# Kernel tuning notes

Hardware: AMD Instinct MI355X
Metric: run time of the kernel (lower is better)

The kernel has to match this reference:

```python
import jax, jax.numpy as jnp
import numpy as np

B, CIN, HW_IN = 128, 3, 32
CONV_OUT, CK = 256, 9
NCAPS, PC, PK, PS = 32, 8, 9, 2
NCAT, DOUT = 10, 16
ROUTING_ITERS = 3
DN = ('NCHW', 'OIHW', 'NCHW')


def setup_inputs() -> dict:
    key = jax.random.key(0)
    ks = jax.random.split(key, 6)
    return {
        "x": jax.random.normal(ks[0], (B, CIN, HW_IN, HW_IN), jnp.float32),
        "conv_w": jax.random.normal(ks[1], (CONV_OUT, CIN, CK, CK), jnp.float32) * 0.05,
        "conv_b": jax.random.normal(ks[2], (CONV_OUT,), jnp.float32) * 0.05,
        "prim_w": jax.random.normal(ks[3], (NCAPS, PC, CONV_OUT, PK, PK), jnp.float32) * 0.05,
        "prim_b": jax.random.normal(ks[4], (NCAPS, PC), jnp.float32) * 0.05,
        "dig_w": jax.random.normal(ks[5], (NCAT, 8 * 8 * NCAPS, PC, DOUT), jnp.float32) * 0.05,
    }


def squash(v):
    s = jnp.sum(v * v, axis=-1, keepdims=True)
    return v * (jnp.sqrt(s) / (1.0 + s))


def reference(x, conv_w, conv_b, prim_w, prim_b, dig_w):
    b = x.shape[0]
    # conv + leaky_relu  -> [B, 256, 24, 24]
    h = jax.lax.conv_general_dilated(x, conv_w, (1, 1), 'VALID', dimension_numbers=DN)
    h = jax.nn.leaky_relu(h + conv_b[None, :, None, None])
    # all 32 primary-cap convs as one conv with 32*8 output channels
    w2 = prim_w.reshape(NCAPS * PC, CONV_OUT, PK, PK)
    p = jax.lax.conv_general_dilated(h, w2, (PS, PS), 'VALID', dimension_numbers=DN)
    p = p + prim_b.reshape(-1)[None, :, None, None]          # [B, 32*8, 8, 8]
    hp, wp = p.shape[2], p.shape[3]
    p = p.reshape(b, NCAPS, PC, hp * wp)                      # [B, 32, 8, HW]
    # torch: cat over caps at dim3 -> [B, 8, HW, 32] -> view(B,8,-1) -> transpose(1,2)
    u = p.transpose(0, 3, 1, 2).reshape(b, hp * wp * NCAPS, PC)
    # note: torch flatten order is (HW, cap); transpose(0,2,3,1) gives [B,8,HW,32]
    u = p.transpose(0, 2, 3, 1).reshape(b, PC, hp * wp * NCAPS).transpose(0, 2, 1)
    u = squash(u)                                             # [B, nodes, 8]
    uhat = jnp.einsum('bni,cnid->bcnd', u, dig_w)             # [B, cat, nodes, dout]
    logits = jnp.zeros(uhat.shape[:3] + (1,), uhat.dtype)
    for _ in range(ROUTING_ITERS):
        probs = jax.nn.softmax(logits, axis=1)
        out = squash(jnp.sum(uhat * probs, axis=2))           # [B, cat, dout]
        logits = logits + jnp.sum(uhat * out[:, :, None, :], axis=3, keepdims=True)
    probs = jax.nn.softmax(logits, axis=1)
    return squash(jnp.sum(uhat * probs, axis=2))              # [B, cat, dout]
```

## Files before the change

kernel.cpp:

```cpp
#include <hip/hip_runtime.h>
#include <hip/hip_bf16.h>

typedef __attribute__((ext_vector_type(8))) short bf16x8;
typedef __attribute__((ext_vector_type(4))) float f32x4;
typedef unsigned short ushort_t;

__device__ inline ushort_t f2bf(float f){
    union { float f; unsigned int u; } v; v.f = f;
    unsigned int r = v.u + 0x7fffu + ((v.u >> 16) & 1u);
    return (ushort_t)(r >> 16);
}

__device__ inline void gload_lds16(const void* g, void* l){
    __builtin_amdgcn_global_load_lds(
        (const __attribute__((address_space(1))) unsigned int*)g,
        (__attribute__((address_space(3))) unsigned int*)l, 16, 0, 0);
}

__global__ __launch_bounds__(256) void k_w2t(const float* __restrict__ pw, ushort_t* __restrict__ w2t)
{
    __shared__ float tile[5184];
    const int oc  = blockIdx.x >> 2;
    const int ic0 = (blockIdx.x & 3) * 64;
    const float* src = pw + (oc*256 + ic0)*81;
    for (int j = threadIdx.x; j < 5184; j += 256) tile[j] = src[j];
    __syncthreads();
    for (int j = threadIdx.x; j < 5184; j += 256){
        int p = j >> 6, ic = j & 63;
        w2t[(oc*81 + p)*256 + ic0 + ic] = f2bf(tile[ic*81 + p]);
    }
}

__global__ __launch_bounds__(256) void k_cwb(const float* __restrict__ cw, ushort_t* __restrict__ cwb){
    const int oc = blockIdx.x;
    const int k  = threadIdx.x;
    cwb[oc*256 + k] = (k < 243) ? f2bf(cw[oc*243 + k]) : (ushort_t)0;
}

__global__ __launch_bounds__(256) void k_conv1m(const float* __restrict__ x,
    const ushort_t* __restrict__ cwb, const float* __restrict__ conv_b,
    ushort_t* __restrict__ ht)
{
    __shared__ ushort_t At[8192];
    __shared__ ushort_t Bt[8192];
    const int tid = threadIdx.x;
    const int bid = blockIdx.x;
    const int mt = bid >> 1, nt = bid & 1;
    const int m0 = mt*128, n0 = nt*128;
    const int lane = tid & 63, wave = tid >> 6;
    const int wm = (wave >> 1)*64, wn = (wave & 1)*64;
    const int l16 = lane & 15, lq = lane >> 4;
    const int rx = l16 & 7;

    int xbase[4], aoff[4], swz[4];
    const ushort_t* bsrc[4];
    #pragma unroll
    for (int t=0;t<4;t++){
        const int cid = tid + t*256;
        const int row = cid >> 3, co = cid & 7;
        swz[t] = (row*8 + (co ^ (row & 7)))*8;
        aoff[t] = co*8;
        const int m = m0 + row;
        const int b = m / 576, rem = m - b*576;
        const int oy = rem / 24, ox = rem - oy*24;
        xbase[t] = b*3072 + oy*32 + ox;
        bsrc[t] = cwb + (n0 + row)*256 + co*8;
    }

    f32x4 acc[4][4];
    #pragma unroll
    for (int i=0;i<4;i++)
        #pragma unroll
        for (int j=0;j<4;j++) acc[i][j] = 0;

    for (int step = 0; step < 4; step++){
        const int k0 = step*64;
        #pragma unroll
        for (int t=0;t<4;t++){
            union { ushort_t u[8]; bf16x8 v; } pk;
            #pragma unroll
            for (int j=0;j<8;j++){
                const int k = k0 + aoff[t] + j;
                float val = 0.f;
                if (k < 243){
                    const int ic = k / 81, p = k - ic*81;
                    const int ky = p / 9, kx = p - ky*9;
                    val = x[xbase[t] + ic*1024 + ky*32 + kx];
                }
                pk.u[j] = f2bf(val);
            }
            *(bf16x8*)&At[swz[t]] = pk.v;
        }
        #pragma unroll
        for (int t=0;t<4;t++){
            bf16x8 v = *(const bf16x8*)(bsrc[t] + k0);
            *(bf16x8*)&Bt[swz[t]] = v;
        }
        __syncthreads();
        #pragma unroll
        for (int kk=0; kk<2; kk++){
            bf16x8 a[4], bb[4];
            const int cs = ((kk*4 + lq) ^ rx)*8;
            #pragma unroll
            for (int f=0; f<4; f++){
                a[f]  = *(const bf16x8*)&At[(wm + f*16 + l16)*64 + cs];
                bb[f] = *(const bf16x8*)&Bt[(wn + f*16 + l16)*64 + cs];
            }
            #pragma unroll
            for (int i=0;i<4;i++)
                #pragma unroll
                for (int j=0;j<4;j++)
                    acc[i][j] = __builtin_amdgcn_mfma_f32_16x16x32_bf16(a[i], bb[j], acc[i][j], 0,0,0);
        }
        __syncthreads();
    }
    #pragma unroll
    for (int j=0;j<4;j++){
        const int n = n0 + wn + j*16 + l16;
        const float bias = conv_b[n];
        #pragma unroll
        for (int i=0;i<4;i++)
            #pragma unroll
            for (int r=0;r<4;r++){
                const int m = m0 + wm + i*16 + lq*4 + r;
                float v = acc[i][j][r] + bias;
                v = v > 0.f ? v : 0.01f*v;
                ht[(size_t)m*256 + n] = f2bf(v);
            }
    }
}

__global__ __launch_bounds__(256) void k_conv2gemm(const ushort_t* __restrict__ ht,
    const ushort_t* __restrict__ w2t, float* __restrict__ p2p)
{
    __shared__ ushort_t At[8192];
    __shared__ ushort_t Bt[8192];
    const int tid = threadIdx.x;
    const int bid = blockIdx.x;
    const int mt = bid & 63, rest = bid >> 6;
    const int nt = rest & 1, ks = rest >> 1;
    const int m0 = mt*128, n0 = nt*128;
    const int lane = tid & 63, wave = tid >> 6;
    const int wm = (wave >> 1)*64, wn = (wave & 1)*64;
    const int l16 = lane & 15, lq = lane >> 4;
    const int rx = l16 & 7;

    const int srow0 = wave*32 + (lane >> 3);
    const int cop = lane & 7;
    const ushort_t* asrc[4];
    const ushort_t* bsrc[4];
    #pragma unroll
    for (int t = 0; t < 4; t++){
        const int row = srow0 + t*8;
        const int col = cop ^ (row & 7);
        const int m = m0 + row;
        const int bi = m >> 6, hw = m & 63;
        const int oy2 = hw >> 3, ox2 = hw & 7;
        asrc[t] = ht + (((bi*24 + 2*oy2)*24) + 2*ox2)*256 + col*8;
        bsrc[t] = w2t + (size_t)(n0 + row)*20736 + col*8;
    }

    f32x4 acc[4][4];
    #pragma unroll
    for (int i=0;i<4;i++)
        #pragma unroll
        for (int j=0;j<4;j++) acc[i][j] = 0;

    const int k_begin = ks*5184;
    for (int step = 0; step < 81; step++){
        const int k0 = k_begin + step*64;
        const int pq = k0 >> 8;
        const int ky = pq/9, kx = pq - ky*9;
        const int aoff = (ky*24 + kx)*256 + (k0 & 255);
        #pragma unroll
        for (int t=0;t<4;t++){
            gload_lds16(asrc[t] + aoff, &At[(wave*4+t)*512]);
            gload_lds16(bsrc[t] + k0,  &Bt[(wave*4+t)*512]);
        }
        __syncthreads();
        #pragma unroll
        for (int kk=0; kk<2; kk++){
            bf16x8 a[4], bb[4];
            const int cs = ((kk*4 + lq) ^ rx)*8;
            #pragma unroll
            for (int f=0; f<4; f++){
                a[f]  = *(const bf16x8*)&At[(wm + f*16 + l16)*64 + cs];
                bb[f] = *(const bf16x8*)&Bt[(wn + f*16 + l16)*64 + cs];
            }
            #pragma unroll
            for (int i=0;i<4;i++)
                #pragma unroll
                for (int j=0;j<4;j++)
                    acc[i][j] = __builtin_amdgcn_mfma_f32_16x16x32_bf16(a[i], bb[j], acc[i][j], 0,0,0);
        }
        __syncthreads();
    }
    float* dst = p2p + (size_t)ks*2097152;
    #pragma unroll
    for (int i=0;i<4;i++)
        #pragma unroll
        for (int j=0;j<4;j++)
            #pragma unroll
            for (int r=0;r<4;r++){
                const int m = m0 + wm + i*16 + lq*4 + r;
                const int n = n0 + wn + j*16 + l16;
                dst[m*256 + n] = acc[i][j][r];
            }
}

__global__ __launch_bounds__(256) void k_squash_u(const float* __restrict__ p2p,
    const float* __restrict__ prim_b, float* __restrict__ u)
{
    const int idx = blockIdx.x*256 + threadIdx.x;
    const int b = idx >> 11, n = idx & 2047;
    const int hw = n >> 5, cap = n & 31;
    const int base = (b*64 + hw)*256 + cap*8;
    float v[8];
    #pragma unroll
    for (int j=0;j<8;j++) v[j] = prim_b[cap*8+j];
    #pragma unroll
    for (int ksp=0; ksp<4; ksp++){
        const float* sp = p2p + (size_t)ksp*2097152 + base;
        #pragma unroll
        for (int j=0;j<8;j++) v[j] += sp[j];
    }
    float s = 0.f;
    #pragma unroll
    for (int j=0;j<8;j++) s += v[j]*v[j];
    const float sc = sqrtf(s)/(1.0f + s);
    float* dst = u + ((size_t)n*128 + b)*8;
    #pragma unroll
    for (int j=0;j<8;j++) dst[j] = v[j]*sc;
}

__global__ __launch_bounds__(256) void k_route9(const float* __restrict__ u_r,
    const float* __restrict__ dw, const float* __restrict__ S,
    float* __restrict__ partials, const int mode)
{
    __shared__ float Wl[5120];
    const int tid = threadIdx.x;
    const int h = tid & 3;
    const int bq = tid >> 2;
    const int n0 = blockIdx.x * 4;
    for (int v = tid; v < 1280; v += 256){
        const int nc = v >> 5, ir = v & 31;
        const int i = ir >> 2, r4 = ir & 3;
        const int n = nc / 10, c = nc - n*10;
        *(f32x4*)&Wl[v*4] =
            *(const f32x4*)(dw + (size_t)(c*2048 + n0 + n)*128 + i*16 + r4*4);
    }
    __syncthreads();

    float oc[2][10][4];
    #pragma unroll
    for (int k=0;k<2;k++)
        #pragma unroll
        for (int c=0;c<10;c++)
            #pragma unroll
            for (int dd=0;dd<4;dd++) oc[k][c][dd] = 0.f;

    #pragma unroll
    for (int n=0;n<4;n++){
        float uu[2][8];
        #pragma unroll
        for (int k=0;k<2;k++){
            const float* up = u_r + ((size_t)(n0+n)*128 + bq + 64*k)*8;
            *(f32x4*)&uu[k][0] = *(const f32x4*)up;
            *(f32x4*)&uu[k][4] = *(const f32x4*)(up+4);
        }
        float ad[2][10][4];
        #pragma unroll
        for (int c=0;c<10;c++){
            const float* wp = &Wl[(n*10+c)*128 + h*4];
            #pragma unroll
            for (int k=0;k<2;k++)
                #pragma unroll
                for (int dd=0;dd<4;dd++) ad[k][c][dd] = 0.f;
            #pragma unroll
            for (int i=0;i<8;i++){
                const f32x4 wv = *(const f32x4*)(wp + i*16);
                #pragma unroll
                for (int k=0;k<2;k++)
                    #pragma unroll
                    for (int dd=0;dd<4;dd++)
                        ad[k][c][dd] = fmaf(wv[dd], uu[k][i], ad[k][c][dd]);
            }
        }
        float p[2][10];
        if (mode){
            #pragma unroll
            for (int k=0;k<2;k++){
                #pragma unroll
                for (int c=0;c<10;c++){
                    const f32x4 sv = *(const f32x4*)(S + (bq+64*k)*160 + c*16 + h*4);
                    float t = ad[k][c][0]*sv[0];
                    t = fmaf(ad[k][c][1], sv[1], t);
                    t = fmaf(ad[k][c][2], sv[2], t);
                    t = fmaf(ad[k][c][3], sv[3], t);
                    t += __shfl_xor(t, 1);
                    t += __shfl_xor(t, 2);
                    p[k][c] = t;
                }
                float mx = p[k][0];
                #pragma unroll
                for (int c=1;c<10;c++) mx = fmaxf(mx, p[k][c]);
                float ssum = 0.f;
                #pragma unroll
                for (int c=0;c<10;c++){ p[k][c] = __expf(p[k][c]-mx); ssum += p[k][c]; }
                const float inv = 1.f/ssum;
                #pragma unroll
                for (int c=0;c<10;c++) p[k][c] *= inv;
            }
        } else {
            #pragma unroll
            for (int k=0;k<2;k++)
                #pragma unroll
                for (int c=0;c<10;c++) p[k][c] = 0.1f;
        }
        #pragma unroll
        for (int k=0;k<2;k++)
            #pragma unroll
            for (int c=0;c<10;c++)
                #pragma unroll
                for (int dd=0;dd<4;dd++)
                    oc[k][c][dd] = fmaf(p[k][c], ad[k][c][dd], oc[k][c][dd]);
    }
    #pragma unroll
    for (int k=0;k<2;k++){
        float* dst = partials + ((size_t)blockIdx.x*128 + bq + 64*k)*160 + h*4;
        #pragma unroll
        for (int c=0;c<10;c++){
            f32x4 v;
            #pragma unroll
            for (int dd=0;dd<4;dd++) v[dd] = oc[k][c][dd];
            *(f32x4*)(dst + c*16) = v;
        }
    }
}

__global__ __launch_bounds__(256) void k_reduce2(const float* __restrict__ partials,
    float* __restrict__ S, float* __restrict__ outp, const int mode)
{
    const int c = blockIdx.x, b = blockIdx.y;
    const int t = threadIdx.x, d = t & 15, g = t >> 4;
    float s = 0.f;
    for (int sl = g; sl < 512; sl += 16)
        s += partials[((size_t)sl*128 + b)*160 + c*16 + d];
    __shared__ float red[256];
    red[t] = s;
    __syncthreads();
    if (g == 0){
        float v = red[d];
        #pragma unroll
        for (int k=1;k<16;k++) v += red[d + k*16];
        float ss = v*v;
        ss += __shfl_xor(ss, 1, 16);
        ss += __shfl_xor(ss, 2, 16);
        ss += __shfl_xor(ss, 4, 16);
        ss += __shfl_xor(ss, 8, 16);
        const float val = v * sqrtf(ss)/(1.f+ss);
        if (mode == 0)      S[b*160 + c*16 + d] = val;
        else if (mode == 1) S[b*160 + c*16 + d] += val;
        else                outp[(b*10 + c)*16 + d] = val;
    }
}

extern "C" void kernel_launch(void* const* d_in, const int* in_sizes, int n_in,
                              void* d_out, int out_size, void* d_ws, size_t ws_size,
                              hipStream_t stream)
{
    const float* x      = (const float*)d_in[0];
    const float* conv_w = (const float*)d_in[1];
    const float* conv_b = (const float*)d_in[2];
    const float* prim_w = (const float*)d_in[3];
    const float* prim_b = (const float*)d_in[4];
    const float* dig_w  = (const float*)d_in[5];
    float* out = (float*)d_out;
    char* ws = (char*)d_ws;

    ushort_t* ht       = (ushort_t*)(ws + 0);
    float*    partials = (float*)   (ws + 0);
    float*    S        = (float*)   (ws + 41943040);
    ushort_t* w2t      = (ushort_t*)(ws + 37748736);
    ushort_t* cwb      = (ushort_t*)(ws + 48365568);
    float*    p2p      = (float*)   (ws + 48614400);
    float*    u        = (float*)   (ws + 82168832);

    k_w2t<<<1024, 256, 0, stream>>>(prim_w, w2t);
    k_cwb<<<256, 256, 0, stream>>>(conv_w, cwb);
    k_conv1m<<<1152, 256, 0, stream>>>(x, cwb, conv_b, ht);
    k_conv2gemm<<<512, 256, 0, stream>>>(ht, w2t, p2p);
    k_squash_u<<<1024, 256, 0, stream>>>(p2p, prim_b, u);

    k_route9<<<512, 256, 0, stream>>>(u, dig_w, S, partials, 0);
    k_reduce2<<<dim3(10,128), 256, 0, stream>>>(partials, S, out, 0);
    k_route9<<<512, 256, 0, stream>>>(u, dig_w, S, partials, 1);
    k_reduce2<<<dim3(10,128), 256, 0, stream>>>(partials, S, out, 1);
    k_route9<<<512, 256, 0, stream>>>(u, dig_w, S, partials, 1);
    k_reduce2<<<dim3(10,128), 256, 0, stream>>>(partials, S, out, 1);
    k_route9<<<512, 256, 0, stream>>>(u, dig_w, S, partials, 1);
    k_reduce2<<<dim3(10,128), 256, 0, stream>>>(partials, S, out, 2);
}
```

Baseline: 369.2 us.

## Specialize first routing pass into dedicated kernel and store routing partials as bf16

The first routing iteration uses uniform probabilities, so it is split into a dedicated kernel that sums uhat over nodes per category and then scales by 0.1 before squashing, with fewer partials to reduce. The remaining routing passes write their per-block partial sums as bf16 instead of fp32, which halves the partial traffic written by route9 and read by the reduction. This adds bf16 rounding error to the accumulated partial sums, which may affect accuracy.

```diff
diff --git a/kernel.cpp b/kernel.cpp
--- a/kernel.cpp
+++ b/kernel.cpp
@@ -4,11 +4,15 @@
 typedef __attribute__((ext_vector_type(8))) short bf16x8;
 typedef __attribute__((ext_vector_type(4))) float f32x4;
 typedef unsigned short ushort_t;
+typedef __attribute__((ext_vector_type(4))) unsigned short ush4;
 
 __device__ inline ushort_t f2bf(float f){
     union { float f; unsigned int u; } v; v.f = f;
     unsigned int r = v.u + 0x7fffu + ((v.u >> 16) & 1u);
     return (ushort_t)(r >> 16);
+}
+__device__ inline float bf2f(ushort_t u){
+    union { unsigned int i; float f; } v; v.i = ((unsigned int)u) << 16; return v.f;
 }
 
 __device__ inline void gload_lds16(const void* g, void* l){
@@ -233,9 +237,72 @@
     for (int j=0;j<8;j++) dst[j] = v[j]*sc;
 }
 
+__global__ __launch_bounds__(128) void k_uhat0(const float* __restrict__ u_r,
+    const float* __restrict__ dw, float* __restrict__ part0)
+{
+    __shared__ float Wl[4096];
+    const int tid = threadIdx.x;
+    const int c = blockIdx.x, ns = blockIdx.y;
+    const int n0 = ns*32;
+    const float* wsrc = dw + (size_t)(c*2048 + n0)*128;
+    for (int s = tid; s < 1024; s += 128)
+        *(f32x4*)&Wl[s*4] = *(const f32x4*)(wsrc + s*4);
+    __syncthreads();
+    const int bg = tid >> 2, dq = tid & 3;
+    float acc[4][4];
+    #pragma unroll
+    for (int kb=0;kb<4;kb++)
+        #pragma unroll
+        for (int dd=0;dd<4;dd++) acc[kb][dd] = 0.f;
+    for (int n = 0; n < 32; n++){
+        float uu[4][8];
+        const float* up = u_r + ((size_t)(n0+n)*128 + bg*4)*8;
+        #pragma unroll
+        for (int kb=0;kb<4;kb++){
+            *(f32x4*)&uu[kb][0] = *(const f32x4*)(up + kb*8);
+            *(f32x4*)&uu[kb][4] = *(const f32x4*)(up + kb*8 + 4);
+        }
+        #pragma unroll
+        for (int i=0;i<8;i++){
+            const f32x4 wv = *(const f32x4*)&Wl[n*128 + i*16 + dq*4];
+            #pragma unroll
+            for (int kb=0;kb<4;kb++)
+                #pragma unroll
+                for (int dd=0;dd<4;dd++)
+                    acc[kb][dd] = fmaf(wv[dd], uu[kb][i], acc[kb][dd]);
+        }
+    }
+    #pragma unroll
+    for (int kb=0;kb<4;kb++){
+        f32x4 v;
+        #pragma unroll
+        for (int dd=0;dd<4;dd++) v[dd] = acc[kb][dd];
+        *(f32x4*)(part0 + ((size_t)ns*128 + bg*4+kb)*160 + c*16 + dq*4) = v;
+    }
+}
+
+__global__ __launch_bounds__(192) void k_red0(const float* __restrict__ part0,
+    float* __restrict__ S)
+{
+    const int b = blockIdx.x;
+    const int t = threadIdx.x;
+    if (t >= 160) return;
+    float s = 0.f;
+    const float* base = part0 + (size_t)b*160 + t;
+    #pragma unroll 8
+    for (int ns=0; ns<64; ns++) s += base[(size_t)ns*20480];
+    s *= 0.1f;
+    float ss = s*s;
+    ss += __shfl_xor(ss, 1, 16);
+    ss += __shfl_xor(ss, 2, 16);
+    ss += __shfl_xor(ss, 4, 16);
+    ss += __shfl_xor(ss, 8, 16);
+    S[b*160 + t] = s * sqrtf(ss)/(1.f+ss);
+}
+
 __global__ __launch_bounds__(256) void k_route9(const float* __restrict__ u_r,
     const float* __restrict__ dw, const float* __restrict__ S,
-    float* __restrict__ partials, const int mode)
+    ushort_t* __restrict__ partials)
 {
     __shared__ float Wl[5120];
     const int tid = threadIdx.x;
@@ -287,35 +354,28 @@
             }
         }
         float p[2][10];
-        if (mode){
-            #pragma unroll
-            for (int k=0;k<2;k++){
-                #pragma unroll
-                for (int c=0;c<10;c++){
-                    const f32x4 sv = *(const f32x4*)(S + (bq+64*k)*160 + c*16 + h*4);
-                    float t = ad[k][c][0]*sv[0];
-                    t = fmaf(ad[k][c][1], sv[1], t);
-                    t = fmaf(ad[k][c][2], sv[2], t);
-                    t = fmaf(ad[k][c][3], sv[3], t);
-                    t += __shfl_xor(t, 1);
-                    t += __shfl_xor(t, 2);
-                    p[k][c] = t;
-                }
-                float mx = p[k][0];
-                #pragma unroll
-                for (int c=1;c<10;c++) mx = fmaxf(mx, p[k][c]);
-                float ssum = 0.f;
-                #pragma unroll
-                for (int c=0;c<10;c++){ p[k][c] = __expf(p[k][c]-mx); ssum += p[k][c]; }
-                const float inv = 1.f/ssum;
-                #pragma unroll
-                for (int c=0;c<10;c++) p[k][c] *= inv;
-            }
-        } else {
-            #pragma unroll
-            for (int k=0;k<2;k++)
-                #pragma unroll
-                for (int c=0;c<10;c++) p[k][c] = 0.1f;
+        #pragma unroll
+        for (int k=0;k<2;k++){
+            #pragma unroll
+            for (int c=0;c<10;c++){
+                const f32x4 sv = *(const f32x4*)(S + (bq+64*k)*160 + c*16 + h*4);
+                float t = ad[k][c][0]*sv[0];
+                t = fmaf(ad[k][c][1], sv[1], t);
+                t = fmaf(ad[k][c][2], sv[2], t);
+                t = fmaf(ad[k][c][3], sv[3], t);
+                t += __shfl_xor(t, 1);
+                t += __shfl_xor(t, 2);
+                p[k][c] = t;
+            }
+            float mx = p[k][0];
+            #pragma unroll
+            for (int c=1;c<10;c++) mx = fmaxf(mx, p[k][c]);
+            float ssum = 0.f;
+            #pragma unroll
+            for (int c=0;c<10;c++){ p[k][c] = __expf(p[k][c]-mx); ssum += p[k][c]; }
+            const float inv = 1.f/ssum;
+            #pragma unroll
+            for (int c=0;c<10;c++) p[k][c] *= inv;
         }
         #pragma unroll
         for (int k=0;k<2;k++)
@@ -327,25 +387,25 @@
     }
     #pragma unroll
     for (int k=0;k<2;k++){
-        float* dst = partials + ((size_t)blockIdx.x*128 + bq + 64*k)*160 + h*4;
+        ushort_t* dst = partials + ((size_t)blockIdx.x*128 + bq + 64*k)*160 + h*4;
         #pragma unroll
         for (int c=0;c<10;c++){
-            f32x4 v;
-            #pragma unroll
-            for (int dd=0;dd<4;dd++) v[dd] = oc[k][c][dd];
-            *(f32x4*)(dst + c*16) = v;
-        }
-    }
-}
-
-__global__ __launch_bounds__(256) void k_reduce2(const float* __restrict__ partials,
+            ush4 v;
+            #pragma unroll
+            for (int dd=0;dd<4;dd++) v[dd] = f2bf(oc[k][c][dd]);
+            *(ush4*)(dst + c*16) = v;
+        }
+    }
+}
+
+__global__ __launch_bounds__(256) void k_reduce2h(const ushort_t* __restrict__ partials,
     float* __restrict__ S, float* __restrict__ outp, const int mode)
 {
     const int c = blockIdx.x, b = blockIdx.y;
     const int t = threadIdx.x, d = t & 15, g = t >> 4;
     float s = 0.f;
     for (int sl = g; sl < 512; sl += 16)
-        s += partials[((size_t)sl*128 + b)*160 + c*16 + d];
+        s += bf2f(partials[((size_t)sl*128 + b)*160 + c*16 + d]);
     __shared__ float red[256];
     red[t] = s;
     __syncthreads();
@@ -359,9 +419,8 @@
         ss += __shfl_xor(ss, 4, 16);
         ss += __shfl_xor(ss, 8, 16);
         const float val = v * sqrtf(ss)/(1.f+ss);
-        if (mode == 0)      S[b*160 + c*16 + d] = val;
-        else if (mode == 1) S[b*160 + c*16 + d] += val;
-        else                outp[(b*10 + c)*16 + d] = val;
+        if (mode == 1) S[b*160 + c*16 + d] += val;
+        else           outp[(b*10 + c)*16 + d] = val;
     }
 }
 
@@ -379,7 +438,8 @@
     char* ws = (char*)d_ws;
 
     ushort_t* ht       = (ushort_t*)(ws + 0);
-    float*    partials = (float*)   (ws + 0);
+    float*    part0    = (float*)   (ws + 0);
+    ushort_t* partials = (ushort_t*)(ws + 0);
     float*    S        = (float*)   (ws + 41943040);
     ushort_t* w2t      = (ushort_t*)(ws + 37748736);
     ushort_t* cwb      = (ushort_t*)(ws + 48365568);
@@ -392,12 +452,12 @@
     k_conv2gemm<<<512, 256, 0, stream>>>(ht, w2t, p2p);
     k_squash_u<<<1024, 256, 0, stream>>>(p2p, prim_b, u);
 
-    k_route9<<<512, 256, 0, stream>>>(u, dig_w, S, partials, 0);
-    k_reduce2<<<dim3(10,128), 256, 0, stream>>>(partials, S, out, 0);
-    k_route9<<<512, 256, 0, stream>>>(u, dig_w, S, partials, 1);
-    k_reduce2<<<dim3(10,128), 256, 0, stream>>>(partials, S, out, 1);
-    k_route9<<<512, 256, 0, stream>>>(u, dig_w, S, partials, 1);
-    k_reduce2<<<dim3(10,128), 256, 0, stream>>>(partials, S, out, 1);
-    k_route9<<<512, 256, 0, stream>>>(u, dig_w, S, partials, 1);
-    k_reduce2<<<dim3(10,128), 256, 0, stream>>>(partials, S, out, 2);
-}
+    k_uhat0<<<dim3(10,64), 128, 0, stream>>>(u, dig_w, part0);
+    k_red0<<<128, 192, 0, stream>>>(part0, S);
+    k_route9<<<512, 256, 0, stream>>>(u, dig_w, S, partials);
+    k_reduce2h<<<dim3(10,128), 256, 0, stream>>>(partials, S, out, 1);
+    k_route9<<<512, 256, 0, stream>>>(u, dig_w, S, partials);
+    k_reduce2h<<<dim3(10,128), 256, 0, stream>>>(partials, S, out, 1);
+    k_route9<<<512, 256, 0, stream>>>(u, dig_w, S, partials);
+    k_reduce2h<<<dim3(10,128), 256, 0, stream>>>(partials, S, out, 2);
+}
```

Result: no change. 369.4 us (+0.1%).
